# Performance work log

Measured on AMD Instinct MI355X. Metric: run time of the kernel, lower is better.

## Reference

```python
import jax, jax.numpy as jnp
import numpy as np

B, SEQ, D = 2, 1024, 768
E, H = 8, 3072          # num_experts, expert hidden (mlp_ratio=4)
CAPACITY = 2            # k = CAPACITY * num_tokens


def setup_inputs() -> dict:
    key = jax.random.key(0)
    ks = jax.random.split(key, 6)
    x = jax.random.normal(ks[0], (B, SEQ, D), dtype=jnp.float32)
    gate_weight = jax.random.normal(ks[1], (E, D), dtype=jnp.float32) * 0.006
    w1 = jax.random.normal(ks[2], (E, D, H), dtype=jnp.float32) * (1.0 / np.sqrt(D))
    b1 = jnp.zeros((E, H), dtype=jnp.float32)
    w2 = jax.random.normal(ks[3], (E, H, D), dtype=jnp.float32) * (1.0 / np.sqrt(H))
    b2 = jnp.zeros((E, D), dtype=jnp.float32)
    return {"x": x, "gate_weight": gate_weight, "w1": w1, "b1": b1, "w2": w2, "b2": b2}


def reference(x, gate_weight, w1, b1, w2, b2):
    Bb, s, d = x.shape
    xf = x.reshape(-1, d)                     # [S, D]
    S = xf.shape[0]
    k = S * CAPACITY
    logits = xf @ gate_weight.T               # [S, E]
    scores = jax.nn.softmax(logits, axis=-1).T  # [E, S]
    # flattened top-k over all (expert, token) pairs -> sparse gate matrix
    vals, idx = jax.lax.top_k(scores.reshape(-1), k)
    gate = jnp.zeros((E * S,), dtype=x.dtype).at[idx].add(vals).reshape(E, S)
    # expert MLPs (GELU-tanh) applied per expert; zero gate entries kill
    # non-routed (expert, token) pairs -> same math as gather/MLP/scatter.
    h = jax.nn.gelu(jnp.einsum('sd,edh->esh', xf, w1) + b1[:, None, :], approximate=True)
    out = jnp.einsum('esh,ehd->esd', h, w2) + b2[:, None, :]   # [E, S, D]
    y = jnp.einsum('es,esd->sd', gate, out)    # weighted combine + sum over experts
    return y.reshape(Bb, s, d)
```

## Files before the change

kernel.cpp:

```cpp
#include <hip/hip_runtime.h>
#include <math.h>

#define S_TOK 2048
#define NEXP  8
#define DDIM  768
#define HDIM  3072
#define KSEL  4096

typedef __attribute__((ext_vector_type(8))) short short8;
typedef __attribute__((ext_vector_type(4))) float f32x4;
typedef __attribute__((ext_vector_type(2))) unsigned int u32x2;

__device__ __forceinline__ unsigned short f2bf(float f) {
  unsigned u = __float_as_uint(f);
  u += 0x7fffu + ((u >> 16) & 1u);
  return (unsigned short)(u >> 16);
}

__device__ __forceinline__ float gelu_fast(float v) {
  float u = 0.7978845608028654f * (v + 0.044715f * v * v * v);
  float t = __expf(-2.0f * fabsf(u));
  float th = (1.0f - t) / (1.0f + t);
  th = copysignf(th, u);
  return 0.5f * v * (1.0f + th);
}

__global__ __launch_bounds__(256) void convx_kernel(const float* __restrict__ x,
                                                    short* __restrict__ xb) {
  int i = (blockIdx.x * 256 + threadIdx.x) * 8;
  float4 a = *(const float4*)(x + i);
  float4 b = *(const float4*)(x + i + 4);
  short8 v;
  v[0] = (short)f2bf(a.x); v[1] = (short)f2bf(a.y);
  v[2] = (short)f2bf(a.z); v[3] = (short)f2bf(a.w);
  v[4] = (short)f2bf(b.x); v[5] = (short)f2bf(b.y);
  v[6] = (short)f2bf(b.z); v[7] = (short)f2bf(b.w);
  *(short8*)(xb + i) = v;
}

__global__ __launch_bounds__(256) void gate_kernel(
    const float* __restrict__ x, const float* __restrict__ gw,
    float* __restrict__ scores)
{
  int tid  = threadIdx.x;
  int lane = tid & 63;
  int wid  = tid >> 6;
  int token = blockIdx.x * 4 + wid;
  const float* xr = x + (size_t)token * DDIM;

  float acc[NEXP];
#pragma unroll
  for (int e = 0; e < NEXP; ++e) acc[e] = 0.f;

  for (int d = lane; d < DDIM; d += 64) {
    float xv = xr[d];
#pragma unroll
    for (int e = 0; e < NEXP; ++e) acc[e] += xv * gw[e * DDIM + d];
  }
#pragma unroll
  for (int e = 0; e < NEXP; ++e) {
    for (int off = 32; off; off >>= 1) acc[e] += __shfl_down(acc[e], off, 64);
  }
  if (lane == 0) {
    float m = acc[0];
#pragma unroll
    for (int e = 1; e < NEXP; ++e) m = fmaxf(m, acc[e]);
    float p[NEXP], s = 0.f;
#pragma unroll
    for (int e = 0; e < NEXP; ++e) { p[e] = expf(acc[e] - m); s += p[e]; }
    float inv = 1.0f / s;
#pragma unroll
    for (int e = 0; e < NEXP; ++e) scores[e * S_TOK + token] = p[e] * inv;
  }
}

__device__ unsigned block_scan_excl(unsigned v, volatile unsigned* wsum) {
  int tid = threadIdx.x, lane = tid & 63, wid = tid >> 6;
  __syncthreads();
  unsigned x = v;
#pragma unroll
  for (int off = 1; off < 64; off <<= 1) {
    unsigned t = __shfl_up(x, off, 64);
    if (lane >= off) x += t;
  }
  if (lane == 63) wsum[wid] = x;
  __syncthreads();
  if (tid < 64) {
    unsigned w = (lane < 16) ? wsum[lane] : 0u;
#pragma unroll
    for (int off = 1; off < 16; off <<= 1) {
      unsigned t = __shfl_up(w, off, 64);
      if (lane >= off) w += t;
    }
    if (lane < 16) wsum[lane] = w;
  }
  __syncthreads();
  unsigned woff = (wid > 0) ? wsum[wid - 1] : 0u;
  return woff + (x - v);
}

__global__ __launch_bounds__(1024) void select_kernel(
    const float* __restrict__ scores,
    int* __restrict__ tokenlist, float* __restrict__ slotgate,
    int* __restrict__ offsets, int* __restrict__ posmap)
{
  __shared__ unsigned cnt;
  __shared__ unsigned wsum[16];
  int tid = threadIdx.x;
  int base = tid * 16;

  float sv[16]; unsigned key[16];
#pragma unroll
  for (int j = 0; j < 16; ++j) {
    sv[j] = scores[base + j];
    key[j] = __float_as_uint(sv[j]);
  }

  unsigned lo = 0, hi = 0x3F800000u;
  while (lo < hi) {
    unsigned mid = lo + ((hi - lo + 1) >> 1);
    if (tid == 0) cnt = 0;
    __syncthreads();
    unsigned c = 0;
#pragma unroll
    for (int j = 0; j < 16; ++j) c += (key[j] >= mid) ? 1u : 0u;
    for (int off = 32; off; off >>= 1) c += __shfl_down(c, off, 64);
    if ((tid & 63) == 0) atomicAdd(&cnt, c);
    __syncthreads();
    unsigned tot = cnt;
    __syncthreads();
    if (tot >= (unsigned)KSEL) lo = mid; else hi = mid - 1;
  }
  unsigned V = lo;

  if (tid == 0) cnt = 0;
  __syncthreads();
  {
    unsigned c = 0;
#pragma unroll
    for (int j = 0; j < 16; ++j) c += (key[j] > V) ? 1u : 0u;
    for (int off = 32; off; off >>= 1) c += __shfl_down(c, off, 64);
    if ((tid & 63) == 0) atomicAdd(&cnt, c);
  }
  __syncthreads();
  int need = KSEL - (int)cnt;
  __syncthreads();

  unsigned tloc = 0;
#pragma unroll
  for (int j = 0; j < 16; ++j) tloc += (key[j] == V) ? 1u : 0u;
  unsigned texcl = block_scan_excl(tloc, wsum);

  unsigned selmask = 0, sloc = 0, trun = texcl;
#pragma unroll
  for (int j = 0; j < 16; ++j) {
    bool f;
    if (key[j] > V) f = true;
    else if (key[j] == V) { f = ((int)trun < need); ++trun; }
    else f = false;
    if (f) { selmask |= (1u << j); ++sloc; }
  }
  unsigned sexcl = block_scan_excl(sloc, wsum);

  if ((tid & 127) == 0) offsets[tid >> 7] = (int)sexcl;
  if (tid == 0) offsets[NEXP] = KSEL;

  unsigned p = sexcl;
#pragma unroll
  for (int j = 0; j < 16; ++j) {
    int i = base + j;
    if (selmask & (1u << j)) {
      posmap[i] = (int)p;
      tokenlist[p] = i & (S_TOK - 1);
      slotgate[p] = sv[j];
      ++p;
    } else {
      posmap[i] = -1;
    }
  }
}

template <int MODE>
__global__ __launch_bounds__(256) void moe_mfma(
    const short* __restrict__ Abase, const float* __restrict__ W,
    const float* __restrict__ bias, void* __restrict__ outp,
    const int* __restrict__ offsets, const int* __restrict__ tokenlist)
{
  const int e = (int)blockIdx.x;
  const int K = (MODE == 1) ? DDIM : HDIM;
  const int N = (MODE == 1) ? HDIM : DDIM;
  const int tile  = (MODE == 1) ? (int)blockIdx.z : ((int)blockIdx.z >> 1);
  const int split = (MODE == 1) ? 0 : ((int)blockIdx.z & 1);
  const int klen  = (MODE == 1) ? DDIM : (HDIM / 2);
  const int kb = split * klen;

  const int r0 = offsets[e];
  const int rows = offsets[e + 1] - r0;
  const int rowbase = tile << 7;
  if (rowbase >= rows) return;
  int vr = rows - rowbase; if (vr > 128) vr = 128;
  const int colbase = (int)blockIdx.y << 7;

  __shared__ short As[128 * 40];
  __shared__ __align__(16) short Bs[32 * 128];
  const unsigned bs_lds = (unsigned)(uintptr_t)&Bs[0];

  const int tid = threadIdx.x;
  const int lane = tid & 63;
  const int wid = tid >> 6;
  const int wr = (wid >> 1) << 6;
  const int wc = (wid & 1) << 6;
  const int l15 = lane & 15;
  const int lq = lane >> 4;

  const int ar = tid >> 1;
  const int ak = (tid & 1) << 4;
  const short* arow;
  {
    int cr = (ar < vr) ? ar : (vr - 1);
    if (MODE == 1) arow = Abase + (size_t)tokenlist[r0 + rowbase + cr] * DDIM;
    else           arow = Abase + (size_t)(r0 + rowbase + cr) * HDIM + kb;
  }

  const int sk = tid >> 3;
  const int g8 = tid & 7;
  const float* wsrc = W + (size_t)e * K * N + (size_t)kb * N + colbase + g8 * 16;
  short* bwr = (short*)Bs + ((((sk >> 2) << 3) + g8) << 6) + ((sk & 3) << 4);

  f32x4 acc[4][4];
#pragma unroll
  for (int i = 0; i < 4; ++i)
#pragma unroll
    for (int j = 0; j < 4; ++j) acc[i][j] = (f32x4){0.f, 0.f, 0.f, 0.f};

  short8 avA0, avA1;
  float4 bw[4];
  {
    avA0 = *(const short8*)(arow + ak);
    avA1 = *(const short8*)(arow + ak + 8);
    const float* wp = wsrc + (size_t)sk * N;
#pragma unroll
    for (int q = 0; q < 4; ++q) bw[q] = *(const float4*)(wp + 4 * q);
  }

#pragma unroll 1
  for (int k0 = 0; k0 < klen; k0 += 32) {
    __syncthreads();
    *(short8*)&As[ar * 40 + ak] = avA0;
    *(short8*)&As[ar * 40 + ak + 8] = avA1;
#pragma unroll
    for (int q = 0; q < 4; ++q) {
      u32x2 pk;
      pk[0] = (unsigned)f2bf(bw[q].x) | ((unsigned)f2bf(bw[q].y) << 16);
      pk[1] = (unsigned)f2bf(bw[q].z) | ((unsigned)f2bf(bw[q].w) << 16);
      *(u32x2*)(bwr + 4 * q) = pk;
    }
    __syncthreads();
    if (k0 + 32 < klen) {
      avA0 = *(const short8*)(arow + k0 + 32 + ak);
      avA1 = *(const short8*)(arow + k0 + 32 + ak + 8);
      const float* wp = wsrc + (size_t)(k0 + 32 + sk) * N;
#pragma unroll
      for (int q = 0; q < 4; ++q) bw[q] = *(const float4*)(wp + 4 * q);
    }
    short8 af[4], bfr[4];
#pragma unroll
    for (int i = 0; i < 4; ++i)
      af[i] = *(const short8*)&As[(wr + i * 16 + l15) * 40 + lq * 8];
#pragma unroll
    for (int j = 0; j < 4; ++j) {
      unsigned off = bs_lds + ((unsigned)((lq << 4) + (wc >> 4) + j) << 7) +
                     ((unsigned)l15 << 3);
      union { short8 s; u32x2 u[2]; } fb;
      asm volatile("ds_read_b64_tr_b16 %0, %2 offset:0\n\t"
                   "ds_read_b64_tr_b16 %1, %2 offset:1024"
                   : "=&v"(fb.u[0]), "=&v"(fb.u[1]) : "v"(off));
      bfr[j] = fb.s;
    }
    asm volatile("s_waitcnt lgkmcnt(0)" ::: "memory");
    __builtin_amdgcn_sched_barrier(0);
#pragma unroll
    for (int i = 0; i < 4; ++i)
#pragma unroll
      for (int j = 0; j < 4; ++j)
        acc[i][j] = __builtin_amdgcn_mfma_f32_16x16x32_bf16(af[i], bfr[j], acc[i][j], 0, 0, 0);
  }

  if (MODE == 1) {
    short* hb = (short*)outp;
    const float* bp = bias + (size_t)e * N + colbase;
#pragma unroll
    for (int i = 0; i < 4; ++i) {
      int rb = wr + i * 16 + lq * 4;
#pragma unroll
      for (int j = 0; j < 4; ++j) {
        int col = wc + j * 16 + l15;
        float bvv = bp[col];
#pragma unroll
        for (int p = 0; p < 4; ++p) {
          int r = rb + p;
          if (r < vr)
            hb[(size_t)(r0 + rowbase + r) * HDIM + colbase + col] =
                (short)f2bf(gelu_fast(acc[i][j][p] + bvv));
        }
      }
    }
  } else {
    float* ob = (float*)outp + (size_t)split * KSEL * DDIM;
    const float* bp = bias + (size_t)e * N + colbase;
#pragma unroll
    for (int i = 0; i < 4; ++i) {
      int rb = wr + i * 16 + lq * 4;
#pragma unroll
      for (int p = 0; p < 4; ++p) {
        int r = rb + p;
        if (r < vr) {
          float* orow = ob + (size_t)(r0 + rowbase + r) * DDIM + colbase;
#pragma unroll
          for (int j = 0; j < 4; ++j) {
            int col = wc + j * 16 + l15;
            orow[col] = acc[i][j][p] + (split == 0 ? bp[col] : 0.f);
          }
        }
      }
    }
  }
}

__global__ __launch_bounds__(256) void combine_kernel(
    const float* __restrict__ outbuf, const int* __restrict__ posmap,
    const float* __restrict__ slotgate, float* __restrict__ y)
{
  int s = blockIdx.x;
  int tid = threadIdx.x;
  float a0 = 0.f, a1 = 0.f, a2 = 0.f;
#pragma unroll
  for (int e = 0; e < NEXP; ++e) {
    int p = posmap[e * S_TOK + s];
    if (p >= 0) {
      float g = slotgate[p];
      const float* o0 = outbuf + (size_t)p * DDIM;
      const float* o1 = outbuf + ((size_t)KSEL + p) * DDIM;
      a0 += g * (o0[tid] + o1[tid]);
      a1 += g * (o0[tid + 256] + o1[tid + 256]);
      a2 += g * (o0[tid + 512] + o1[tid + 512]);
    }
  }
  float* yr = y + (size_t)s * DDIM;
  yr[tid] = a0;
  yr[tid + 256] = a1;
  yr[tid + 512] = a2;
}

extern "C" void kernel_launch(void* const* d_in, const int* in_sizes, int n_in,
                              void* d_out, int out_size, void* d_ws, size_t ws_size,
                              hipStream_t stream) {
  const float* x  = (const float*)d_in[0];
  const float* gw = (const float*)d_in[1];
  const float* w1 = (const float*)d_in[2];
  const float* b1 = (const float*)d_in[3];
  const float* w2 = (const float*)d_in[4];
  const float* b2 = (const float*)d_in[5];
  float* y = (float*)d_out;

  char* ws = (char*)d_ws;
  float* scores    = (float*)(ws);
  int*   tokenlist = (int*)(ws + (64 << 10));
  float* slotgate  = (float*)(ws + (80 << 10));
  int*   offsets   = (int*)(ws + (96 << 10));
  int*   posmap    = (int*)(ws + (128 << 10));
  short* xbf       = (short*)(ws + (192 << 10));
  short* hbuf      = (short*)(ws + (192 << 10) + (size_t)S_TOK * DDIM * 2);
  float* outbuf    = (float*)(ws + (192 << 10) + (size_t)S_TOK * DDIM * 2
                                  + (size_t)KSEL * HDIM * 2);

  convx_kernel<<<S_TOK * DDIM / 2048, 256, 0, stream>>>(x, xbf);
  gate_kernel<<<S_TOK / 4, 256, 0, stream>>>(x, gw, scores);
  select_kernel<<<1, 1024, 0, stream>>>(scores, tokenlist, slotgate, offsets, posmap);

  dim3 g1(NEXP, HDIM / 128, 16);
  moe_mfma<1><<<g1, 256, 0, stream>>>(xbf, w1, b1, hbuf, offsets, tokenlist);
  dim3 g2(NEXP, DDIM / 128, 32);
  moe_mfma<2><<<g2, 256, 0, stream>>>(hbuf, w2, b2, outbuf, offsets, tokenlist);

  combine_kernel<<<S_TOK, 256, 0, stream>>>(outbuf, posmap, slotgate, y);
}
```

Before: 196.1 us.

## Double-buffer LDS tiles in expert GEMM to halve barriers per k-step

```diff
diff --git a/kernel.cpp b/kernel.cpp
--- a/kernel.cpp
+++ b/kernel.cpp
@@ -201,9 +201,12 @@
   int vr = rows - rowbase; if (vr > 128) vr = 128;
   const int colbase = (int)blockIdx.y << 7;
 
-  __shared__ short As[128 * 40];
-  __shared__ __align__(16) short Bs[32 * 128];
-  const unsigned bs_lds = (unsigned)(uintptr_t)&Bs[0];
+  __shared__ short As0[128 * 40];
+  __shared__ short As1[128 * 40];
+  __shared__ __align__(16) short Bs0[32 * 128];
+  __shared__ __align__(16) short Bs1[32 * 128];
+  const unsigned bs0_lds = (unsigned)(uintptr_t)&Bs0[0];
+  const unsigned bs1_lds = (unsigned)(uintptr_t)&Bs1[0];
 
   const int tid = threadIdx.x;
   const int lane = tid & 63;
@@ -225,7 +228,7 @@
   const int sk = tid >> 3;
   const int g8 = tid & 7;
   const float* wsrc = W + (size_t)e * K * N + (size_t)kb * N + colbase + g8 * 16;
-  short* bwr = (short*)Bs + ((((sk >> 2) << 3) + g8) << 6) + ((sk & 3) << 4);
+  const int bwoff = ((((sk >> 2) << 3) + g8) << 6) + ((sk & 3) << 4);
 
   f32x4 acc[4][4];
 #pragma unroll
@@ -233,57 +236,71 @@
 #pragma unroll
     for (int j = 0; j < 4; ++j) acc[i][j] = (f32x4){0.f, 0.f, 0.f, 0.f};
 
-  short8 avA0, avA1;
-  float4 bw[4];
-  {
-    avA0 = *(const short8*)(arow + ak);
-    avA1 = *(const short8*)(arow + ak + 8);
-    const float* wp = wsrc + (size_t)sk * N;
-#pragma unroll
-    for (int q = 0; q < 4; ++q) bw[q] = *(const float4*)(wp + 4 * q);
-  }
+  short8 avP0, avP1, avQ0, avQ1;
+  float4 bwP[4], bwQ[4];
+
+#define LOAD_AB(A0, A1, BW, KN)                                  \
+  {                                                              \
+    A0 = *(const short8*)(arow + (KN) + ak);                     \
+    A1 = *(const short8*)(arow + (KN) + ak + 8);                 \
+    const float* wp = wsrc + (size_t)((KN) + sk) * N;            \
+    _Pragma("unroll")                                            \
+    for (int q = 0; q < 4; ++q) BW[q] = *(const float4*)(wp + 4 * q); \
+  }
+
+#define WRITE_LDS(A0, A1, BW, AS, BS)                            \
+  {                                                              \
+    *(short8*)&AS[ar * 40 + ak] = A0;                            \
+    *(short8*)&AS[ar * 40 + ak + 8] = A1;                        \
+    _Pragma("unroll")                                            \
+    for (int q = 0; q < 4; ++q) {                                \
+      u32x2 pk;                                                  \
+      pk[0] = (unsigned)f2bf(BW[q].x) | ((unsigned)f2bf(BW[q].y) << 16); \
+      pk[1] = (unsigned)f2bf(BW[q].z) | ((unsigned)f2bf(BW[q].w) << 16); \
+      *(u32x2*)((short*)BS + bwoff + 4 * q) = pk;                \
+    }                                                            \
+  }
+
+#define FRAGS_MFMA(AS, BLDS)                                     \
+  {                                                              \
+    short8 af[4], bfr[4];                                        \
+    _Pragma("unroll")                                            \
+    for (int i = 0; i < 4; ++i)                                  \
+      af[i] = *(const short8*)&AS[(wr + i * 16 + l15) * 40 + lq * 8]; \
+    _Pragma("unroll")                                            \
+    for (int j = 0; j < 4; ++j) {                                \
+      unsigned off = (BLDS) + ((unsigned)((lq << 4) + (wc >> 4) + j) << 7) + \
+                     ((unsigned)l15 << 3);                       \
+      union { short8 s; u32x2 u[2]; } fb;                        \
+      asm volatile("ds_read_b64_tr_b16 %0, %2 offset:0\n\t"      \
+                   "ds_read_b64_tr_b16 %1, %2 offset:1024"       \
+                   : "=&v"(fb.u[0]), "=&v"(fb.u[1]) : "v"(off)); \
+      bfr[j] = fb.s;                                             \
+    }                                                            \
+    asm volatile("s_waitcnt lgkmcnt(0)" ::: "memory");           \
+    __builtin_amdgcn_sched_barrier(0);                           \
+    _Pragma("unroll")                                            \
+    for (int i = 0; i < 4; ++i)                                  \
+      _Pragma("unroll")                                          \
+      for (int j = 0; j < 4; ++j)                                \
+        acc[i][j] = __builtin_amdgcn_mfma_f32_16x16x32_bf16(af[i], bfr[j], acc[i][j], 0, 0, 0); \
+  }
+
+  LOAD_AB(avP0, avP1, bwP, 0);
+  WRITE_LDS(avP0, avP1, bwP, As0, Bs0);
+  LOAD_AB(avQ0, avQ1, bwQ, 32);
+  __syncthreads();
 
 #pragma unroll 1
-  for (int k0 = 0; k0 < klen; k0 += 32) {
+  for (int k0 = 0; k0 < klen; k0 += 64) {
+    if (k0 + 64 < klen) LOAD_AB(avP0, avP1, bwP, k0 + 64);
+    FRAGS_MFMA(As0, bs0_lds);
+    WRITE_LDS(avQ0, avQ1, bwQ, As1, Bs1);
     __syncthreads();
-    *(short8*)&As[ar * 40 + ak] = avA0;
-    *(short8*)&As[ar * 40 + ak + 8] = avA1;
-#pragma unroll
-    for (int q = 0; q < 4; ++q) {
-      u32x2 pk;
-      pk[0] = (unsigned)f2bf(bw[q].x) | ((unsigned)f2bf(bw[q].y) << 16);
-      pk[1] = (unsigned)f2bf(bw[q].z) | ((unsigned)f2bf(bw[q].w) << 16);
-      *(u32x2*)(bwr + 4 * q) = pk;
-    }
+    if (k0 + 96 < klen) LOAD_AB(avQ0, avQ1, bwQ, k0 + 96);
+    FRAGS_MFMA(As1, bs1_lds);
+    if (k0 + 64 < klen) { WRITE_LDS(avP0, avP1, bwP, As0, Bs0); }
     __syncthreads();
-    if (k0 + 32 < klen) {
-      avA0 = *(const short8*)(arow + k0 + 32 + ak);
-      avA1 = *(const short8*)(arow + k0 + 32 + ak + 8);
-      const float* wp = wsrc + (size_t)(k0 + 32 + sk) * N;
-#pragma unroll
-      for (int q = 0; q < 4; ++q) bw[q] = *(const float4*)(wp + 4 * q);
-    }
-    short8 af[4], bfr[4];
-#pragma unroll
-    for (int i = 0; i < 4; ++i)
-      af[i] = *(const short8*)&As[(wr + i * 16 + l15) * 40 + lq * 8];
-#pragma unroll
-    for (int j = 0; j < 4; ++j) {
-      unsigned off = bs_lds + ((unsigned)((lq << 4) + (wc >> 4) + j) << 7) +
-                     ((unsigned)l15 << 3);
-      union { short8 s; u32x2 u[2]; } fb;
-      asm volatile("ds_read_b64_tr_b16 %0, %2 offset:0\n\t"
-                   "ds_read_b64_tr_b16 %1, %2 offset:1024"
-                   : "=&v"(fb.u[0]), "=&v"(fb.u[1]) : "v"(off));
-      bfr[j] = fb.s;
-    }
-    asm volatile("s_waitcnt lgkmcnt(0)" ::: "memory");
-    __builtin_amdgcn_sched_barrier(0);
-#pragma unroll
-    for (int i = 0; i < 4; ++i)
-#pragma unroll
-      for (int j = 0; j < 4; ++j)
-        acc[i][j] = __builtin_amdgcn_mfma_f32_16x16x32_bf16(af[i], bfr[j], acc[i][j], 0, 0, 0);
   }
 
   if (MODE == 1) {
```

Measured after the change: 197.3 us. About the same (+0.6%).
